# Optimization experiments

Hardware: AMD Instinct MI355X
Metric: run time of the kernel (lower is better)

The kernel has to match this reference:

```python
import jax, jax.numpy as jnp
import numpy as np

D = 128          # voxel grid resolution per axis
N = 500_000      # number of active voxels
C = 64           # channels (in == out)
K = 27           # 3x3x3 kernel volume
EPS = 1e-5


def _build_geometry():
    """Random active voxel set + submanifold 3x3x3 neighbor index pairs."""
    rng = np.random.default_rng(0)
    lin = rng.choice(D ** 3, size=N, replace=False).astype(np.int64)
    zc, yc, xc = lin // (D * D), (lin // D) % D, lin % D
    order = np.argsort(lin)
    sorted_lin = lin[order]
    nbr = np.zeros((K, N), np.int32)
    valid = np.zeros((K, N), np.float32)
    k = 0
    for dz in (-1, 0, 1):
        for dy in (-1, 0, 1):
            for dx in (-1, 0, 1):
                nz, ny, nx = zc + dz, yc + dy, xc + dx
                inb = (nz >= 0) & (nz < D) & (ny >= 0) & (ny < D) & (nx >= 0) & (nx < D)
                nlin = nz * D * D + ny * D + nx
                pos = np.clip(np.searchsorted(sorted_lin, nlin), 0, N - 1)
                found = inb & (sorted_lin[pos] == nlin)
                nbr[k] = np.where(found, order[pos], 0).astype(np.int32)
                valid[k] = found.astype(np.float32)
                k += 1
    return jnp.asarray(nbr), jnp.asarray(valid)


def setup_inputs() -> dict:
    key = jax.random.key(0)
    k_feat, k_w1, k_w2 = jax.random.split(key, 3)
    nbr_idx, valid = _build_geometry()
    scale = 1.0 / np.sqrt(K * C)  # kaiming-ish fan-in init
    return {
        "features": jax.random.normal(k_feat, (N, C), jnp.float32),
        "nbr_idx": nbr_idx,
        "valid": valid,
        "W1": jax.random.normal(k_w1, (K, C, C), jnp.float32) * scale,
        "gamma1": jnp.ones((C,), jnp.float32),
        "beta1": jnp.zeros((C,), jnp.float32),
        "W2": jax.random.normal(k_w2, (K, C, C), jnp.float32) * scale,
        "gamma2": jnp.ones((C,), jnp.float32),
        "beta2": jnp.zeros((C,), jnp.float32),
    }


def _subm_conv(x, W, nbr_idx, valid):
    """Submanifold 3D conv as gather-GEMM-accumulate over K kernel offsets."""
    def step(acc, kw):
        Wk, nk, vk = kw
        return acc + (x[nk] * vk[:, None]) @ Wk, None  # [N,Cin] @ [Cin,Cout]
    acc0 = jnp.zeros((x.shape[0], W.shape[-1]), x.dtype)
    acc, _ = jax.lax.scan(step, acc0, (W, nbr_idx, valid))
    return acc


def _batchnorm(f, gamma, beta):
    """Training-mode BN over active voxels (biased variance, like torch)."""
    mean = jnp.mean(f, axis=0)
    var = jnp.mean(jnp.square(f - mean), axis=0)
    return (f - mean) * jax.lax.rsqrt(var + EPS) * gamma + beta


def reference(features, nbr_idx, valid, W1, gamma1, beta1, W2, gamma2, beta2):
    out = _subm_conv(features, W1, nbr_idx, valid)
    out = jax.nn.relu(_batchnorm(out, gamma1, beta1))
    out = _subm_conv(out, W2, nbr_idx, valid)
    out = _batchnorm(out, gamma2, beta2)
    return jax.nn.relu(out + features)  # identity shortcut (Cin==Cout, stride=1)
```

## Files before the change

kernel.cpp:

```cpp
#include <hip/hip_runtime.h>
#include <hip/hip_bf16.h>
#include <stdint.h>

typedef __attribute__((ext_vector_type(8))) short short8;
typedef __attribute__((ext_vector_type(4))) float floatx4;

__device__ __forceinline__ float bf2f(unsigned short u) {
    union { unsigned int ui; float f; } v; v.ui = ((unsigned int)u) << 16; return v.f;
}
__device__ __forceinline__ unsigned short f2bf(float f) {
    union { float f; unsigned int u; } v; v.f = f;
    unsigned int u = v.u;
    unsigned int r = (u + 0x7fffu + ((u >> 16) & 1u)) >> 16;
    return (unsigned short)r;
}

__global__ __launch_bounds__(256)
void convert_bf16(const float* __restrict__ in, unsigned short* __restrict__ out, int n4) {
    int i = blockIdx.x * blockDim.x + threadIdx.x;
    int stride = gridDim.x * blockDim.x;
    for (; i < n4; i += stride) {
        float4 v = ((const float4*)in)[i];
        ushort4 o;
        o.x = f2bf(v.x); o.y = f2bf(v.y); o.z = f2bf(v.z); o.w = f2bf(v.w);
        ((ushort4*)out)[i] = o;
    }
}

__global__ __launch_bounds__(256)
void encode_kernel(const int* __restrict__ nbr, const float* __restrict__ valid,
                   int* __restrict__ enc, int nvox, int nvoxp) {
    int k = blockIdx.y;
    int r = blockIdx.x * 256 + threadIdx.x;
    int v = -1;
    if (r < nvox) {
        float f = valid[(size_t)k * nvox + r];
        int ix = nbr[(size_t)k * nvox + r];
        v = (f != 0.f) ? ix : -1;
    }
    enc[(size_t)k * nvoxp + r] = v;
}

__global__ __launch_bounds__(256)
void pack_w(const float* __restrict__ W1, const float* __restrict__ W2,
            unsigned short* __restrict__ Wp1, unsigned short* __restrict__ Wp2) {
    int bi = blockIdx.x;
    const float* W = (bi < 27) ? W1 : W2;
    unsigned short* Wp = (bi < 27) ? Wp1 : Wp2;
    int kk = bi % 27;
    int t = threadIdx.x;
    int lane = t & 63, grp = t >> 6;
    int q = lane >> 4, l15 = lane & 15;
    for (int c8 = grp; c8 < 8; c8 += 4) {
        int ks = c8 >> 2, nt = c8 & 3;
        unsigned short* dst = Wp + (((kk*2 + ks)*4 + nt)*64 + lane)*8;
        const float* src = W + kk*4096 + (ks*32 + q*8)*64 + nt*16 + l15;
        #pragma unroll
        for (int j = 0; j < 8; ++j) dst[j] = f2bf(src[j*64]);
    }
}

__global__ __launch_bounds__(256, 4)
void conv_kernel(const unsigned short* __restrict__ xin, const int* __restrict__ enc,
                 const unsigned short* __restrict__ Wp, const unsigned short* __restrict__ zrow,
                 unsigned short* __restrict__ yout, float* __restrict__ sums,
                 int nvox, int nvoxp) {
    __shared__ float sred[128];
    int t = threadIdx.x;
    int wave = t >> 6, lane = t & 63;
    int q = lane >> 4, l15 = lane & 15;
    int m0 = blockIdx.x * 128 + wave * 32;
    int qb = q * 8;

    if (t < 128) sred[t] = 0.f;
    __syncthreads();

    floatx4 acc[2][4];
    #pragma unroll
    for (int s = 0; s < 2; ++s)
        #pragma unroll
        for (int nt = 0; nt < 4; ++nt) acc[s][nt] = (floatx4){0.f, 0.f, 0.f, 0.f};

    short8 avA[2][2], avB[2][2];
    short8 bv[2][4];
    int esA[2], esB[2];

    const int* encL = enc + m0 + l15;

#define ESLOAD(esX, kkv) { int kc_ = (kkv) > 26 ? 26 : (kkv); \
    const int* ep_ = encL + kc_ * nvoxp; \
    esX[0] = ep_[0]; esX[1] = ep_[16]; }

#define GATHER(avX, esX) { _Pragma("unroll") for (int s_ = 0; s_ < 2; ++s_) { \
    const unsigned short* rp_ = (esX[s_] >= 0) ? (xin + ((size_t)(unsigned)esX[s_] << 6)) : zrow; \
    avX[0][s_] = *(const short8*)(rp_ + qb); \
    avX[1][s_] = *(const short8*)(rp_ + 32 + qb); } }

#define BLOAD(kkv) { const unsigned short* wq_ = Wp + (kkv) * 4096 + lane * 8; \
    _Pragma("unroll") for (int ks_ = 0; ks_ < 2; ++ks_) \
    _Pragma("unroll") for (int nt_ = 0; nt_ < 4; ++nt_) \
        bv[ks_][nt_] = *(const short8*)(wq_ + ks_ * 2048 + nt_ * 512); }

#define MFMA_PHASE(avX) { __builtin_amdgcn_s_setprio(1); \
    _Pragma("unroll") for (int ks_ = 0; ks_ < 2; ++ks_) \
    _Pragma("unroll") for (int nt_ = 0; nt_ < 4; ++nt_) { \
        acc[0][nt_] = __builtin_amdgcn_mfma_f32_16x16x32_bf16(avX[ks_][0], bv[ks_][nt_], acc[0][nt_], 0, 0, 0); \
        acc[1][nt_] = __builtin_amdgcn_mfma_f32_16x16x32_bf16(avX[ks_][1], bv[ks_][nt_], acc[1][nt_], 0, 0, 0); } \
    __builtin_amdgcn_s_setprio(0); }

    ESLOAD(esA, 0);
    ESLOAD(esB, 1);
    GATHER(avA, esA);
    ESLOAD(esA, 2);

    #pragma unroll 1
    for (int kkp = 0; kkp < 26; kkp += 2) {
        BLOAD(kkp);
        __builtin_amdgcn_sched_barrier(0);
        GATHER(avB, esB);
        ESLOAD(esB, kkp + 3);
        __builtin_amdgcn_sched_barrier(0);
        MFMA_PHASE(avA);

        BLOAD(kkp + 1);
        __builtin_amdgcn_sched_barrier(0);
        GATHER(avA, esA);
        ESLOAD(esA, kkp + 4);
        __builtin_amdgcn_sched_barrier(0);
        MFMA_PHASE(avB);
    }
    BLOAD(26);
    __builtin_amdgcn_sched_barrier(0);
    MFMA_PHASE(avA);

#undef ESLOAD
#undef GATHER
#undef BLOAD
#undef MFMA_PHASE

    #pragma unroll
    for (int s = 0; s < 2; ++s) {
        int rowb = m0 + s*16 + q*4;
        #pragma unroll
        for (int r = 0; r < 4; ++r) {
            if (rowb + r < nvox) {
                unsigned short* yo = yout + (size_t)(rowb + r)*64 + l15;
                #pragma unroll
                for (int nt = 0; nt < 4; ++nt)
                    yo[nt*16] = f2bf(acc[s][nt][r]);
            }
        }
    }

    #pragma unroll
    for (int nt = 0; nt < 4; ++nt) {
        float s_ = 0.f, q_ = 0.f;
        #pragma unroll
        for (int s = 0; s < 2; ++s)
            #pragma unroll
            for (int r = 0; r < 4; ++r) {
                float v = acc[s][nt][r];
                s_ += v; q_ += v*v;
            }
        atomicAdd(&sred[nt*16 + l15], s_);
        atomicAdd(&sred[64 + nt*16 + l15], q_);
    }
    __syncthreads();
    if (t < 128) atomicAdd(&sums[t], sred[t]);
}

__global__ void finalize_kernel(const float* __restrict__ sums, const float* __restrict__ gamma,
                                const float* __restrict__ beta, float* __restrict__ ab, float invn) {
    int c = threadIdx.x;
    if (c < 64) {
        float mean = sums[c] * invn;
        float var  = sums[64 + c] * invn - mean*mean;
        float a = gamma[c] * rsqrtf(var + 1e-5f);
        ab[c] = a;
        ab[64 + c] = beta[c] - mean * a;
    }
}

__global__ __launch_bounds__(256)
void bnrelu_kernel(unsigned short* __restrict__ y, const float* __restrict__ ab, int n4) {
    int i = blockIdx.x * blockDim.x + threadIdx.x;
    int stride = gridDim.x * blockDim.x;
    for (; i < n4; i += stride) {
        uint2 v = ((const uint2*)y)[i];
        int c0 = (i*4) & 63;
        float f0 = fmaxf(ab[c0]   * bf2f((unsigned short)(v.x & 0xffffu)) + ab[64 + c0],   0.f);
        float f1 = fmaxf(ab[c0+1] * bf2f((unsigned short)(v.x >> 16))     + ab[64 + c0+1], 0.f);
        float f2 = fmaxf(ab[c0+2] * bf2f((unsigned short)(v.y & 0xffffu)) + ab[64 + c0+2], 0.f);
        float f3 = fmaxf(ab[c0+3] * bf2f((unsigned short)(v.y >> 16))     + ab[64 + c0+3], 0.f);
        uint2 o;
        o.x = (unsigned int)f2bf(f0) | ((unsigned int)f2bf(f1) << 16);
        o.y = (unsigned int)f2bf(f2) | ((unsigned int)f2bf(f3) << 16);
        ((uint2*)y)[i] = o;
    }
}

__global__ __launch_bounds__(256)
void final_kernel(const unsigned short* __restrict__ y2, const float* __restrict__ feat,
                  const float* __restrict__ ab, float* __restrict__ out, int ntot2) {
    int i = blockIdx.x * blockDim.x + threadIdx.x;
    int stride = gridDim.x * blockDim.x;
    for (; i < ntot2; i += stride) {
        unsigned int v = ((const unsigned int*)y2)[i];
        int c0 = (i*2) & 63;
        float2 f = ((const float2*)feat)[i];
        float r0 = fmaxf(ab[c0]   * bf2f((unsigned short)(v & 0xffffu)) + ab[64 + c0]   + f.x, 0.f);
        float r1 = fmaxf(ab[c0+1] * bf2f((unsigned short)(v >> 16))     + ab[64 + c0+1] + f.y, 0.f);
        ((float2*)out)[i] = make_float2(r0, r1);
    }
}

extern "C" void kernel_launch(void* const* d_in, const int* in_sizes, int n_in,
                              void* d_out, int out_size, void* d_ws, size_t ws_size,
                              hipStream_t stream) {
    const float* features = (const float*)d_in[0];
    const int*   nbr      = (const int*)d_in[1];
    const float* valid    = (const float*)d_in[2];
    const float* W1       = (const float*)d_in[3];
    const float* gamma1   = (const float*)d_in[4];
    const float* beta1    = (const float*)d_in[5];
    const float* W2       = (const float*)d_in[6];
    const float* gamma2   = (const float*)d_in[7];
    const float* beta2    = (const float*)d_in[8];
    float* out = (float*)d_out;

    int nvox  = in_sizes[0] / 64;
    int nvoxp = (nvox + 255) & ~255;
    size_t featB = (size_t)nvox * 64 * 2;

    char* ob = (char*)d_out;
    unsigned short* xb = (unsigned short*)ob;
    unsigned short* y1 = (unsigned short*)(ob + featB);

    char* ws = (char*)d_ws;
    float* stats = (float*)ws;
    float* sums1 = stats;
    float* sums2 = stats + 128;
    float* ab1   = stats + 256;
    float* ab2   = stats + 384;
    const unsigned short* zrow = (const unsigned short*)(ws + 2048);
    unsigned short* Wp1 = (unsigned short*)(ws + 4096);
    unsigned short* Wp2 = (unsigned short*)(ws + 4096 + 221184);
    int* enc = (int*)(ws + 524288);
    size_t encB = (size_t)27 * nvoxp * 4;
    unsigned short* y2 = (unsigned short*)(ws + 524288 + encB);

    hipMemsetAsync(ws, 0, 4096, stream);

    convert_bf16<<<2048, 256, 0, stream>>>(features, xb, nvox * 16);
    pack_w<<<54, 256, 0, stream>>>(W1, W2, Wp1, Wp2);
    dim3 eg(nvoxp / 256, 27);
    encode_kernel<<<eg, 256, 0, stream>>>(nbr, valid, enc, nvox, nvoxp);

    int convGrid = nvoxp / 128;
    conv_kernel<<<convGrid, 256, 0, stream>>>(xb, enc, Wp1, zrow, y1, sums1, nvox, nvoxp);
    finalize_kernel<<<1, 64, 0, stream>>>(sums1, gamma1, beta1, ab1, 1.0f / nvox);
    bnrelu_kernel<<<2048, 256, 0, stream>>>(y1, ab1, nvox * 16);
    conv_kernel<<<convGrid, 256, 0, stream>>>(y1, enc, Wp2, zrow, y2, sums2, nvox, nvoxp);
    finalize_kernel<<<1, 64, 0, stream>>>(sums2, gamma2, beta2, ab2, 1.0f / nvox);
    final_kernel<<<4096, 256, 0, stream>>>(y2, features, ab2, out, nvox * 32);
}
```

Baseline: 837.2 us.

## Stage conv weights in double-buffered LDS and double rows per wave

Each wave now computes 64 rows instead of 32, and the block covers 256 voxels. Per-offset weights are loaded once per block into a double-buffered shared-memory tile and read from LDS for the MFMAs, instead of every wave loading them from global memory into registers. Block indices are also remapped so consecutive voxel tiles land on the same XCD. The aim is to cut redundant weight traffic and raise MFMA work per gather. In exchange it adds a block barrier per kernel offset, uses more registers (occupancy drops to 3 waves) and halves the grid.

```diff
diff --git a/kernel.cpp b/kernel.cpp
--- a/kernel.cpp
+++ b/kernel.cpp
@@ -60,86 +60,106 @@
     }
 }
 
-__global__ __launch_bounds__(256, 4)
+__global__ __launch_bounds__(256, 3)
 void conv_kernel(const unsigned short* __restrict__ xin, const int* __restrict__ enc,
                  const unsigned short* __restrict__ Wp, const unsigned short* __restrict__ zrow,
                  unsigned short* __restrict__ yout, float* __restrict__ sums,
                  int nvox, int nvoxp) {
+    __shared__ unsigned short wbuf[2][4096];
     __shared__ float sred[128];
+
     int t = threadIdx.x;
     int wave = t >> 6, lane = t & 63;
     int q = lane >> 4, l15 = lane & 15;
-    int m0 = blockIdx.x * 128 + wave * 32;
     int qb = q * 8;
 
+    int nwg = gridDim.x;
+    int q8 = nwg >> 3, r8 = nwg & 7;
+    int xcd = blockIdx.x & 7, jj = blockIdx.x >> 3;
+    int bswz = (xcd < r8 ? xcd * (q8 + 1) : r8 * (q8 + 1) + (xcd - r8) * q8) + jj;
+
+    int m0 = bswz * 256 + wave * 64;
+
     if (t < 128) sred[t] = 0.f;
-    __syncthreads();
-
-    floatx4 acc[2][4];
+
+    floatx4 acc[4][4];
     #pragma unroll
-    for (int s = 0; s < 2; ++s)
+    for (int s = 0; s < 4; ++s)
         #pragma unroll
         for (int nt = 0; nt < 4; ++nt) acc[s][nt] = (floatx4){0.f, 0.f, 0.f, 0.f};
 
-    short8 avA[2][2], avB[2][2];
-    short8 bv[2][4];
-    int esA[2], esB[2];
+    short8 avA[2][4], avB[2][4];
+    uint4 wl0, wl1;
+    int esA[4], esB[4];
 
     const int* encL = enc + m0 + l15;
 
 #define ESLOAD(esX, kkv) { int kc_ = (kkv) > 26 ? 26 : (kkv); \
     const int* ep_ = encL + kc_ * nvoxp; \
-    esX[0] = ep_[0]; esX[1] = ep_[16]; }
-
-#define GATHER(avX, esX) { _Pragma("unroll") for (int s_ = 0; s_ < 2; ++s_) { \
+    esX[0] = ep_[0]; esX[1] = ep_[16]; esX[2] = ep_[32]; esX[3] = ep_[48]; }
+
+#define GATHER(avX, esX) { _Pragma("unroll") for (int s_ = 0; s_ < 4; ++s_) { \
     const unsigned short* rp_ = (esX[s_] >= 0) ? (xin + ((size_t)(unsigned)esX[s_] << 6)) : zrow; \
     avX[0][s_] = *(const short8*)(rp_ + qb); \
     avX[1][s_] = *(const short8*)(rp_ + 32 + qb); } }
 
-#define BLOAD(kkv) { const unsigned short* wq_ = Wp + (kkv) * 4096 + lane * 8; \
-    _Pragma("unroll") for (int ks_ = 0; ks_ < 2; ++ks_) \
-    _Pragma("unroll") for (int nt_ = 0; nt_ < 4; ++nt_) \
-        bv[ks_][nt_] = *(const short8*)(wq_ + ks_ * 2048 + nt_ * 512); }
-
-#define MFMA_PHASE(avX) { __builtin_amdgcn_s_setprio(1); \
+#define STAGE_LOAD(kkv) { const uint4* wp_ = (const uint4*)(Wp + (kkv) * 4096) + t; \
+    wl0 = wp_[0]; wl1 = wp_[256]; }
+
+#define STAGE_WRITE(bufX) { ((uint4*)(bufX))[t] = wl0; ((uint4*)(bufX))[t + 256] = wl1; }
+
+#define MFMA_PHASE(avX, wb_) { __builtin_amdgcn_s_setprio(1); \
     _Pragma("unroll") for (int ks_ = 0; ks_ < 2; ++ks_) \
     _Pragma("unroll") for (int nt_ = 0; nt_ < 4; ++nt_) { \
-        acc[0][nt_] = __builtin_amdgcn_mfma_f32_16x16x32_bf16(avX[ks_][0], bv[ks_][nt_], acc[0][nt_], 0, 0, 0); \
-        acc[1][nt_] = __builtin_amdgcn_mfma_f32_16x16x32_bf16(avX[ks_][1], bv[ks_][nt_], acc[1][nt_], 0, 0, 0); } \
+        short8 bv_ = *(const short8*)((wb_) + ((ks_ * 4 + nt_) * 64 + lane) * 8); \
+        _Pragma("unroll") for (int s_ = 0; s_ < 4; ++s_) \
+            acc[s_][nt_] = __builtin_amdgcn_mfma_f32_16x16x32_bf16(avX[ks_][s_], bv_, acc[s_][nt_], 0, 0, 0); } \
     __builtin_amdgcn_s_setprio(0); }
+
+#define PIPE_BARRIER() { __builtin_amdgcn_sched_barrier(0); \
+    asm volatile("s_waitcnt lgkmcnt(0)" ::: "memory"); \
+    __builtin_amdgcn_s_barrier(); \
+    __builtin_amdgcn_sched_barrier(0); }
 
     ESLOAD(esA, 0);
     ESLOAD(esB, 1);
+    STAGE_LOAD(0);
     GATHER(avA, esA);
     ESLOAD(esA, 2);
+    STAGE_WRITE(wbuf[0]);
+    PIPE_BARRIER();
 
     #pragma unroll 1
-    for (int kkp = 0; kkp < 26; kkp += 2) {
-        BLOAD(kkp);
-        __builtin_amdgcn_sched_barrier(0);
+    for (int kk = 0; kk < 26; kk += 2) {
+        STAGE_LOAD(kk + 1);
         GATHER(avB, esB);
-        ESLOAD(esB, kkp + 3);
-        __builtin_amdgcn_sched_barrier(0);
-        MFMA_PHASE(avA);
-
-        BLOAD(kkp + 1);
-        __builtin_amdgcn_sched_barrier(0);
+        ESLOAD(esB, kk + 3);
+        __builtin_amdgcn_sched_barrier(0);
+        MFMA_PHASE(avA, wbuf[0]);
+        __builtin_amdgcn_sched_barrier(0);
+        STAGE_WRITE(wbuf[1]);
+        PIPE_BARRIER();
+
+        STAGE_LOAD(kk + 2);
         GATHER(avA, esA);
-        ESLOAD(esA, kkp + 4);
-        __builtin_amdgcn_sched_barrier(0);
-        MFMA_PHASE(avB);
-    }
-    BLOAD(26);
-    __builtin_amdgcn_sched_barrier(0);
-    MFMA_PHASE(avA);
+        ESLOAD(esA, kk + 4);
+        __builtin_amdgcn_sched_barrier(0);
+        MFMA_PHASE(avB, wbuf[1]);
+        __builtin_amdgcn_sched_barrier(0);
+        STAGE_WRITE(wbuf[0]);
+        PIPE_BARRIER();
+    }
+    MFMA_PHASE(avA, wbuf[0]);
 
 #undef ESLOAD
 #undef GATHER
-#undef BLOAD
+#undef STAGE_LOAD
+#undef STAGE_WRITE
 #undef MFMA_PHASE
+#undef PIPE_BARRIER
 
     #pragma unroll
-    for (int s = 0; s < 2; ++s) {
+    for (int s = 0; s < 4; ++s) {
         int rowb = m0 + s*16 + q*4;
         #pragma unroll
         for (int r = 0; r < 4; ++r) {
@@ -156,7 +176,7 @@
     for (int nt = 0; nt < 4; ++nt) {
         float s_ = 0.f, q_ = 0.f;
         #pragma unroll
-        for (int s = 0; s < 2; ++s)
+        for (int s = 0; s < 4; ++s)
             #pragma unroll
             for (int r = 0; r < 4; ++r) {
                 float v = acc[s][nt][r];
@@ -256,7 +276,7 @@
     dim3 eg(nvoxp / 256, 27);
     encode_kernel<<<eg, 256, 0, stream>>>(nbr, valid, enc, nvox, nvoxp);
 
-    int convGrid = nvoxp / 128;
+    int convGrid = nvoxp / 256;
     conv_kernel<<<convGrid, 256, 0, stream>>>(xb, enc, Wp1, zrow, y1, sums1, nvox, nvoxp);
     finalize_kernel<<<1, 64, 0, stream>>>(sums1, gamma1, beta1, ab1, 1.0f / nvox);
     bnrelu_kernel<<<2048, 256, 0, stream>>>(y1, ab1, nvox * 16);
```

Measured after the change: 800.5 us. -4.4%, faster.
